# Optimization experiments

Measured on AMD Instinct MI355X. Metric: run time of the kernel, lower is better.

Reference implementation:

```python
import jax, jax.numpy as jnp
import numpy as np
import math

B, S, D = 4, 2048, 1024
N_HEADS = 16
D_FF = 4096
T_DIM = 256
KEEP_RATIO = 0.7
EPS = 1e-5


def _layernorm(x):
    mu = jnp.mean(x, axis=-1, keepdims=True)
    var = jnp.mean((x - mu) ** 2, axis=-1, keepdims=True)
    return (x - mu) * jax.lax.rsqrt(var + EPS)


def _ada_ln(x, cond, W, b):
    # cond: (B, T_DIM); W: (2D, T_DIM)
    p = jax.nn.silu(cond) @ W.T + b            # (B, 2D)
    gamma, beta = jnp.split(p, 2, axis=-1)
    return _layernorm(x) * (1.0 + gamma[:, None, :]) + beta[:, None, :]


def _mha(h, in_w, in_b, out_w, out_b):
    b, s, d = h.shape
    hd = d // N_HEADS
    qkv = h @ in_w.T + in_b                     # (b, s, 3d)
    q, k, v = jnp.split(qkv, 3, axis=-1)
    def heads(t):
        return t.reshape(b, s, N_HEADS, hd).transpose(0, 2, 1, 3)
    q, k, v = heads(q), heads(k), heads(v)
    scores = jnp.einsum('bhqd,bhkd->bhqk', q, k) / math.sqrt(hd)
    attn = jax.nn.softmax(scores, axis=-1)
    o = jnp.einsum('bhqk,bhkd->bhqd', attn, v)  # (b, h, s, hd)
    o = o.transpose(0, 2, 1, 3).reshape(b, s, d)
    return o @ out_w.T + out_b


def setup_inputs() -> dict:
    key = jax.random.key(0)
    ks = jax.random.split(key, 24)
    sc = 0.02
    return {
        'x': jax.random.normal(ks[0], (B, S, D), jnp.float32),
        't_emb': jax.random.normal(ks[1], (B, T_DIM), jnp.float32),
        'tr_w1': jax.random.normal(ks[2], (32, D), jnp.float32) * sc,
        'tr_b1': jnp.zeros((32,), jnp.float32),
        'tr_w2': jax.random.normal(ks[3], (1, 32), jnp.float32) * sc,
        'tr_b2': jnp.zeros((1,), jnp.float32),
        'ln1_w': jax.random.normal(ks[4], (2 * D, T_DIM), jnp.float32) * sc,
        'ln1_b': jnp.zeros((2 * D,), jnp.float32),
        'ln2_w': jax.random.normal(ks[5], (2 * D, T_DIM), jnp.float32) * sc,
        'ln2_b': jnp.zeros((2 * D,), jnp.float32),
        'in_proj_w': jax.random.normal(ks[6], (3 * D, D), jnp.float32) * sc,
        'in_proj_b': jnp.zeros((3 * D,), jnp.float32),
        'out_w': jax.random.normal(ks[7], (D, D), jnp.float32) * sc,
        'out_b': jnp.zeros((D,), jnp.float32),
        'ffn_w1': jax.random.normal(ks[8], (D_FF, D), jnp.float32) * sc,
        'ffn_b1': jnp.zeros((D_FF,), jnp.float32),
        'ffn_w2': jax.random.normal(ks[9], (D, D_FF), jnp.float32) * sc,
        'ffn_b2': jnp.zeros((D,), jnp.float32),
        # torch inits gates to zero; use small randn so the block is non-trivial
        'gate_attn': jax.random.normal(ks[10], (1, 1, D), jnp.float32) * sc,
        'gate_ffn': jax.random.normal(ks[11], (1, 1, D), jnp.float32) * sc,
    }


def reference(x, t_emb, tr_w1, tr_b1, tr_w2, tr_b2, ln1_w, ln1_b, ln2_w, ln2_b,
              in_proj_w, in_proj_b, out_w, out_b, ffn_w1, ffn_b1, ffn_w2, ffn_b2,
              gate_attn, gate_ffn):
    b, s, d = x.shape
    num_keep = max(int(s * KEEP_RATIO), 1)

    # token importance on detached x (stop_gradient mirrors x.detach())
    xd = jax.lax.stop_gradient(x)
    imp = jax.nn.silu(xd @ tr_w1.T + tr_b1) @ tr_w2.T + tr_b2  # (b, s, 1)
    imp = imp[..., 0]
    _, idx = jax.lax.top_k(imp, num_keep)
    idx = jnp.sort(idx, axis=-1)                               # (b, num_keep)

    x_sel = jnp.take_along_axis(x, idx[..., None], axis=1)     # (b, k, d)

    h = _ada_ln(x_sel, t_emb, ln1_w, ln1_b)
    h = _mha(h, in_proj_w, in_proj_b, out_w, out_b)
    x_sel = x_sel + gate_attn * h

    h = _ada_ln(x_sel, t_emb, ln2_w, ln2_b)
    h = jax.nn.gelu(h @ ffn_w1.T + ffn_b1, approximate=False) @ ffn_w2.T + ffn_b2
    x_sel = x_sel + gate_ffn * h

    batch_idx = jnp.arange(b)[:, None]
    return x.at[batch_idx, idx].set(x_sel)
```

## Files before the change

kernel.cpp:

```cpp
#include <hip/hip_runtime.h>
#include <hip/hip_bf16.h>
#include <cmath>
#include <cstdint>

typedef __bf16 bf16;
typedef __bf16 bf16x8 __attribute__((ext_vector_type(8)));
typedef __bf16 bf16x4 __attribute__((ext_vector_type(4)));
typedef float  f32x4  __attribute__((ext_vector_type(4)));

constexpr int B_   = 4;
constexpr int S_   = 2048;
constexpr int D_   = 1024;
constexpr int H_   = 16;
constexpr int DFF_ = 4096;
constexpr int TD_  = 256;
constexpr int KEEP = 1433;
constexpr int M_TOT = B_ * KEEP;
constexpr int MPAD  = 5888;
constexpr int QT64  = (KEEP + 63) / 64;
constexpr int NKV   = (KEEP + 63) / 64;
constexpr float EPS = 1e-5f;
constexpr float QSCALE = 0.18033688011112042f;

__device__ __forceinline__ f32x4 mfma16(bf16x8 a, bf16x8 b, f32x4 c) {
  return __builtin_amdgcn_mfma_f32_16x16x32_bf16(a, b, c, 0, 0, 0);
}

#define GLOAD_LDS(gp, lp)                                                     \
  __builtin_amdgcn_global_load_lds(                                           \
      (const __attribute__((address_space(1))) void*)(gp),                    \
      (__attribute__((address_space(3))) void*)(lp), 16, 0, 0)

#define FENCE_BARRIER()                                                       \
  do {                                                                        \
    __builtin_amdgcn_sched_barrier(0);                                        \
    __builtin_amdgcn_s_barrier();                                             \
    __builtin_amdgcn_sched_barrier(0);                                        \
  } while (0)

__global__ __launch_bounds__(256) void k_impgemv(
    const float* __restrict__ x, const float* __restrict__ w1,
    double* __restrict__ hidden)
{
  const int lane = threadIdx.x & 63, w = threadIdx.x >> 6;
  const int tok0 = blockIdx.x * 16 + w * 4;
  const int u0 = blockIdx.y * 8;
  const float* xb = x + (size_t)tok0 * D_ + lane * 4;
  const float* wb = w1 + (size_t)u0 * D_ + lane * 4;
  double acc[4][8] = {};
#pragma unroll 2
  for (int c = 0; c < D_; c += 256) {
    float4 xv[4], wv[8];
#pragma unroll
    for (int i = 0; i < 4; ++i)
      xv[i] = *(const float4*)(xb + (size_t)i * D_ + c);
#pragma unroll
    for (int u = 0; u < 8; ++u)
      wv[u] = *(const float4*)(wb + (size_t)u * D_ + c);
#pragma unroll
    for (int i = 0; i < 4; ++i)
#pragma unroll
      for (int u = 0; u < 8; ++u) {
        acc[i][u] += (double)xv[i].x * (double)wv[u].x;
        acc[i][u] += (double)xv[i].y * (double)wv[u].y;
        acc[i][u] += (double)xv[i].z * (double)wv[u].z;
        acc[i][u] += (double)xv[i].w * (double)wv[u].w;
      }
  }
#pragma unroll
  for (int i = 0; i < 4; ++i)
#pragma unroll
    for (int u = 0; u < 8; ++u) {
      double s = acc[i][u];
      for (int o = 32; o > 0; o >>= 1) s += __shfl_xor(s, o);
      acc[i][u] = s;
    }
  if (lane == 0) {
#pragma unroll
    for (int i = 0; i < 4; ++i)
#pragma unroll
      for (int u = 0; u < 8; ++u)
        hidden[(size_t)(tok0 + i) * 32 + u0 + u] = acc[i][u];
  }
}

__global__ __launch_bounds__(256) void k_imptail(
    const double* __restrict__ hidden, const float* __restrict__ b1,
    const float* __restrict__ w2, const float* __restrict__ b2,
    double* __restrict__ imp)
{
  const int tok = blockIdx.x * 256 + threadIdx.x;
  const double* hp = hidden + (size_t)tok * 32;
  double r = 0.0;
#pragma unroll
  for (int u = 0; u < 32; ++u) {
    double s = hp[u] + (double)b1[u];
    double sv = s / (1.0 + exp(-s));
    r += sv * (double)w2[u];
  }
  imp[tok] = r + (double)b2[0];
}

__global__ __launch_bounds__(256) void k_rank(const double* __restrict__ imp,
                                              int* __restrict__ rank)
{
  const int b = blockIdx.x >> 5;
  const int seg = blockIdx.x & 31;
  __shared__ double vals[S_];
  const double* ib = imp + (size_t)b * S_;
  for (int i = threadIdx.x; i < S_ / 2; i += 256)
    ((double2*)vals)[i] = ((const double2*)ib)[i];
  __syncthreads();
  const int tl = threadIdx.x >> 2;
  const int part = threadIdx.x & 3;
  const int s = seg * 64 + tl;
  const double v = vals[s];
  int cnt = 0;
  for (int j = part * 512; j < (part + 1) * 512; ++j) {
    double u = vals[j];
    cnt += (u > v) || (u == v && j < s);
  }
  cnt += __shfl_xor(cnt, 1);
  cnt += __shfl_xor(cnt, 2);
  if (part == 0) rank[b * S_ + s] = cnt;
}

__global__ __launch_bounds__(256) void k_compact(const int* __restrict__ rank,
                                                 int* __restrict__ idx)
{
  const int b = blockIdx.x;
  __shared__ int wcnt[4];
  __shared__ int base_s;
  if (threadIdx.x == 0) base_s = 0;
  __syncthreads();
  const int t = threadIdx.x, lane = t & 63, w = t >> 6;
  for (int c = 0; c < S_ / 256; ++c) {
    const int s = c * 256 + t;
    const bool kept = rank[b * S_ + s] < KEEP;
    unsigned long long m = __ballot(kept);
    int piw = __popcll(m & ((1ull << lane) - 1ull));
    if (lane == 0) wcnt[w] = __popcll(m);
    __syncthreads();
    int off = base_s;
    for (int i = 0; i < w; ++i) off += wcnt[i];
    if (kept) idx[b * KEEP + off + piw] = s;
    __syncthreads();
    if (t == 0) base_s += wcnt[0] + wcnt[1] + wcnt[2] + wcnt[3];
    __syncthreads();
  }
}

__global__ __launch_bounds__(256) void k_condproj(
    const float* __restrict__ temb, const float* __restrict__ W,
    const float* __restrict__ bias, float* __restrict__ p)
{
  const int gw = (int)((blockIdx.x * 256 + threadIdx.x) >> 6);
  const int lane = threadIdx.x & 63;
  const int b = gw >> 11;
  const int row = gw & 2047;
  const float* te = temb + (size_t)b * TD_;
  const float* wr = W + (size_t)row * TD_;
  float acc = 0.f;
  for (int i = lane; i < TD_; i += 64) {
    float c = te[i];
    acc += (c / (1.f + __expf(-c))) * wr[i];
  }
  for (int o = 32; o > 0; o >>= 1) acc += __shfl_down(acc, o);
  if (lane == 0) p[(size_t)b * 2 * D_ + row] = acc + bias[row];
}

__global__ void k_f2b(const float* __restrict__ src, bf16* __restrict__ dst, int n4)
{
  int i = blockIdx.x * 256 + threadIdx.x;
  if (i < n4) {
    float4 v = ((const float4*)src)[i];
    bf16x4 o = {(bf16)v.x, (bf16)v.y, (bf16)v.z, (bf16)v.w};
    ((bf16x4*)dst)[i] = o;
  }
}

__global__ __launch_bounds__(256) void k_adaln(
    const float* __restrict__ xsrc, const int* __restrict__ idx,
    const float* __restrict__ p, bf16* __restrict__ hout)
{
  const int r = blockIdx.x, t = threadIdx.x;
  bf16* orow = hout + (size_t)r * D_;
  if (r >= M_TOT) {
    bf16x4 z = {(bf16)0.f, (bf16)0.f, (bf16)0.f, (bf16)0.f};
    ((bf16x4*)orow)[t] = z;
    return;
  }
  const int b = r / KEEP, j = r - b * KEEP;
  const int s = idx[b * KEEP + j];
  const float* xr = xsrc + ((size_t)(b * S_ + s)) * D_;
  float4 v = ((const float4*)xr)[t];
  __shared__ float red[8];
  float sum = v.x + v.y + v.z + v.w;
  for (int o = 32; o > 0; o >>= 1) sum += __shfl_down(sum, o);
  const int lane = t & 63, w = t >> 6;
  if (lane == 0) red[w] = sum;
  __syncthreads();
  const float mu = (red[0] + red[1] + red[2] + red[3]) * (1.f / D_);
  const float dx = v.x - mu, dy = v.y - mu, dz = v.z - mu, dw = v.w - mu;
  float vs = dx * dx + dy * dy + dz * dz + dw * dw;
  for (int o = 32; o > 0; o >>= 1) vs += __shfl_down(vs, o);
  if (lane == 0) red[4 + w] = vs;
  __syncthreads();
  const float rstd = rsqrtf((red[4] + red[5] + red[6] + red[7]) * (1.f / D_) + EPS);
  const float* gp = p + (size_t)b * 2 * D_;
  float4 g  = ((const float4*)gp)[t];
  float4 be = ((const float4*)(gp + D_))[t];
  bf16x4 o;
  o[0] = (bf16)(dx * rstd * (1.f + g.x) + be.x);
  o[1] = (bf16)(dy * rstd * (1.f + g.y) + be.y);
  o[2] = (bf16)(dz * rstd * (1.f + g.z) + be.z);
  o[3] = (bf16)(dw * rstd * (1.f + g.w) + be.w);
  ((bf16x4*)orow)[t] = o;
}

template <int BN, int MODE>
__global__ __launch_bounds__(256) void k_gemm(
    const bf16* __restrict__ A, const bf16* __restrict__ W,
    const float* __restrict__ bias, bf16* __restrict__ Cbf,
    const float* __restrict__ gate, const int* __restrict__ idx,
    float* __restrict__ resid, int N, int K, int gn)
{
  constexpr int WN = BN / 2;
  constexpr int NJ = WN / 16;
  __shared__ bf16 As[2][128 * 64];
  __shared__ bf16 Ws[2][BN * 64];
  const int t = threadIdx.x, lane = t & 63;
  const int w = t >> 6, wr = w >> 1, wc = w & 1;
  const int fr = lane & 15, fq = lane >> 4;

  const int nwg = gridDim.x, orig = blockIdx.x;
  const int q8 = nwg >> 3, r8 = nwg & 7;
  const int xc = orig & 7, pos = orig >> 3;
  const int wgid = (xc < r8 ? xc * (q8 + 1) : r8 * (q8 + 1) + (xc - r8) * q8) + pos;
  const int bm = wgid / gn, bn = wgid - bm * gn;

  const bf16* Ab = A + (size_t)bm * 128 * K;
  const bf16* Wb = W + (size_t)bn * BN * K;

  auto stage = [&](int buf, int kt) {
    const int ko = kt * 64;
#pragma unroll
    for (int it = 0; it < 4; ++it) {
      const int e = it * 256 + t;
      const int row = e >> 3, pc = e & 7;
      const int lc = pc ^ (row & 7);
      GLOAD_LDS(Ab + (size_t)row * K + ko + lc * 8, &As[buf][0] + e * 8);
    }
#pragma unroll
    for (int it = 0; it < BN / 32; ++it) {
      const int e = it * 256 + t;
      const int row = e >> 3, pc = e & 7;
      const int lc = pc ^ (row & 7);
      GLOAD_LDS(Wb + (size_t)row * K + ko + lc * 8, &Ws[buf][0] + e * 8);
    }
  };

  f32x4 acc[4][NJ] = {};
  stage(0, 0);
  const int nkt = K >> 6;
  int cur = 0;
  for (int kt = 0; kt < nkt; ++kt) {
    __syncthreads();
    if (kt + 1 < nkt) stage(cur ^ 1, kt + 1);
    const char* Al = (const char*)&As[cur][0];
    const char* Wl = (const char*)&Ws[cur][0];
#pragma unroll
    for (int kk = 0; kk < 2; ++kk) {
      bf16x8 af[4], wf[NJ];
#pragma unroll
      for (int i = 0; i < 4; ++i)
        af[i] = *(const bf16x8*)(Al + (wr * 64 + i * 16 + fr) * 128 +
                                 (((kk * 4 + fq) ^ (fr & 7)) << 4));
#pragma unroll
      for (int j = 0; j < NJ; ++j)
        wf[j] = *(const bf16x8*)(Wl + (wc * WN + j * 16 + fr) * 128 +
                                 (((kk * 4 + fq) ^ (fr & 7)) << 4));
#pragma unroll
      for (int i = 0; i < 4; ++i)
#pragma unroll
        for (int j = 0; j < NJ; ++j)
          acc[i][j] = mfma16(af[i], wf[j], acc[i][j]);
    }
    cur ^= 1;
  }

#pragma unroll
  for (int i = 0; i < 4; ++i) {
#pragma unroll
    for (int j = 0; j < NJ; ++j) {
#pragma unroll
      for (int r = 0; r < 4; ++r) {
        const int m = bm * 128 + wr * 64 + i * 16 + fq * 4 + r;
        const int n = bn * BN + wc * WN + j * 16 + fr;
        float v = acc[i][j][r] + bias[n];
        if (MODE == 0) {
          if (n < D_) v *= QSCALE;
          Cbf[(size_t)m * N + n] = (bf16)v;
        } else if (MODE == 1) {
          float gl = 0.5f * v * (1.f + erff(v * 0.70710678118654752f));
          Cbf[(size_t)m * N + n] = (bf16)gl;
        } else {
          if (m < M_TOT) {
            const int b = m / KEEP, jj = m - b * KEEP;
            const int s = idx[b * KEEP + jj];
            resid[((size_t)(b * S_ + s)) * D_ + n] += gate[n] * v;
          }
        }
      }
    }
  }
}

template <int MODE>
__global__ __launch_bounds__(512) void k_gemm256(
    const bf16* __restrict__ A, const bf16* __restrict__ W,
    const float* __restrict__ bias, bf16* __restrict__ Cbf, int N, int K, int gn)
{
  __shared__ bf16 As[2][256 * 64];
  __shared__ bf16 Ws[2][256 * 64];
  const int t = threadIdx.x, lane = t & 63;
  const int wid = t >> 6, wr = wid >> 2, wc = wid & 3;
  const int fr = lane & 15, fq = lane >> 4;

  const int nwg = gridDim.x, orig = blockIdx.x;
  const int q8 = nwg >> 3, r8 = nwg & 7;
  const int xc = orig & 7, pos = orig >> 3;
  const int wgid = (xc < r8 ? xc * (q8 + 1) : r8 * (q8 + 1) + (xc - r8) * q8) + pos;
  const int bm = wgid / gn, bn = wgid - bm * gn;

  const bf16* Ab = A + (size_t)bm * 256 * K;
  const bf16* Wb = W + (size_t)bn * 256 * K;

  const bf16* pA[4];
  const bf16* pW[4];
#pragma unroll
  for (int it = 0; it < 4; ++it) {
    const int e = it * 512 + t;
    const int row = e >> 3, pc = e & 7;
    const int lc = pc ^ (row & 7);
    pA[it] = Ab + (size_t)row * K + lc * 8;
    pW[it] = Wb + (size_t)row * K + lc * 8;
  }

  auto stage = [&](int buf) {
#pragma unroll
    for (int it = 0; it < 4; ++it) {
      const int e = it * 512 + t;
      GLOAD_LDS(pA[it], &As[buf][0] + e * 8);
      pA[it] += 64;
    }
#pragma unroll
    for (int it = 0; it < 4; ++it) {
      const int e = it * 512 + t;
      GLOAD_LDS(pW[it], &Ws[buf][0] + e * 8);
      pW[it] += 64;
    }
  };

  f32x4 acc[8][4] = {};
  stage(0);
  stage(1);
  const int nkt = K >> 6;

  for (int kt = 0; kt < nkt; ++kt) {
    if (kt < nkt - 1) {
      asm volatile("s_waitcnt vmcnt(8)" ::: "memory");
    } else {
      asm volatile("s_waitcnt vmcnt(0)" ::: "memory");
    }
    FENCE_BARRIER();
    const int c = kt & 1;
    const char* Al = (const char*)&As[c][0];
    const char* Wl = (const char*)&Ws[c][0];
#pragma unroll
    for (int kk = 0; kk < 2; ++kk) {
      bf16x8 af[8], wf[4];
      const int pcsel = ((kk * 4 + fq) ^ (fr & 7)) << 4;
#pragma unroll
      for (int i = 0; i < 8; ++i)
        af[i] = *(const bf16x8*)(Al + (wr * 128 + i * 16 + fr) * 128 + pcsel);
#pragma unroll
      for (int j = 0; j < 4; ++j)
        wf[j] = *(const bf16x8*)(Wl + (wc * 64 + j * 16 + fr) * 128 + pcsel);
      __builtin_amdgcn_s_setprio(1);
#pragma unroll
      for (int i = 0; i < 8; ++i)
#pragma unroll
        for (int j = 0; j < 4; ++j)
          acc[i][j] = mfma16(af[i], wf[j], acc[i][j]);
      __builtin_amdgcn_s_setprio(0);
    }
    FENCE_BARRIER();
    if (kt + 2 < nkt) stage(c);
  }

#pragma unroll
  for (int i = 0; i < 8; ++i) {
#pragma unroll
    for (int j = 0; j < 4; ++j) {
#pragma unroll
      for (int r = 0; r < 4; ++r) {
        const int m = bm * 256 + wr * 128 + i * 16 + fq * 4 + r;
        const int n = bn * 256 + wc * 64 + j * 16 + fr;
        float v = acc[i][j][r] + bias[n];
        if (MODE == 0) {
          if (n < D_) v *= QSCALE;
          Cbf[(size_t)m * N + n] = (bf16)v;
        } else {
          float gl = 0.5f * v * (1.f + erff(v * 0.70710678118654752f));
          Cbf[(size_t)m * N + n] = (bf16)gl;
        }
      }
    }
  }
}

__global__ __launch_bounds__(256) void k_attn(const bf16* __restrict__ qkv,
                                              bf16* __restrict__ out)
{
  __shared__ bf16 Klds[2][64 * 64];
  __shared__ bf16 Vlds[2][64 * 64];

  const int t = threadIdx.x;
  const int lane = t & 63, w = t >> 6;
  const int fr = lane & 15, fq = lane >> 4;
  const int qt = blockIdx.x, h = blockIdx.y, b = blockIdx.z;
  const size_t rowbase = (size_t)b * KEEP;
  const size_t RS = 3 * D_;
  const bf16* kbase = qkv + rowbase * RS + D_ + h * 64;
  const bf16* vbase = qkv + rowbase * RS + 2 * D_ + h * 64;

  const int wq0 = qt * 64 + w * 16;
  const int qrow = min(wq0 + fr, KEEP - 1);
  const bf16* qp = qkv + (rowbase + qrow) * RS + h * 64 + fq * 8;
  const bf16x8 qf0 = *(const bf16x8*)qp;
  const bf16x8 qf1 = *(const bf16x8*)(qp + 32);

  f32x4 o[4] = {};
  float mrow = -INFINITY, lrow = 0.f;

  const int p0 = t, p1 = 256 + t;
  auto kaddr = [&](int p, int kv) {
    const int row = p >> 3, c8p = p & 7;
    const int c8 = c8p ^ ((row & 7) ^ (row >> 3));
    const int gr = min(kv + row, KEEP - 1);
    return kbase + (size_t)gr * RS + c8 * 8;
  };
  auto vaddr = [&](int p, int kv) {
    const int db = p >> 7, ksub = (p >> 3) & 15, jr = (p >> 1) & 3,
              c8lo = p & 1;
    const int vrow = ksub * 4 + jr, vc8 = db * 2 + c8lo;
    const int gr = min(kv + vrow, KEEP - 1);
    return vbase + (size_t)gr * RS + vc8 * 8;
  };
  const bf16* kp0 = kaddr(p0, 0);
  const bf16* kp1 = kaddr(p1, 0);
  const bf16* vp0 = vaddr(p0, 0);
  const bf16* vp1 = vaddr(p1, 0);

  auto stage_fast = [&](int buf) {
    GLOAD_LDS(kp0, &Klds[buf][0] + p0 * 8);
    GLOAD_LDS(kp1, &Klds[buf][0] + p1 * 8);
    GLOAD_LDS(vp0, &Vlds[buf][0] + p0 * 8);
    GLOAD_LDS(vp1, &Vlds[buf][0] + p1 * 8);
    kp0 += 64 * RS; kp1 += 64 * RS; vp0 += 64 * RS; vp1 += 64 * RS;
  };
  auto stage_last = [&](int buf, int kv) {
    GLOAD_LDS(kaddr(p0, kv), &Klds[buf][0] + p0 * 8);
    GLOAD_LDS(kaddr(p1, kv), &Klds[buf][0] + p1 * 8);
    GLOAD_LDS(vaddr(p0, kv), &Vlds[buf][0] + p0 * 8);
    GLOAD_LDS(vaddr(p1, kv), &Vlds[buf][0] + p1 * 8);
  };

  stage_fast(0);
  int cur = 0;

  const unsigned vbase_lds0 =
      (unsigned)(size_t)(__attribute__((address_space(3))) bf16*)&Vlds[0][0];
  const unsigned vbase_lds1 =
      (unsigned)(size_t)(__attribute__((address_space(3))) bf16*)&Vlds[1][0];

  for (int ti = 0; ti < NKV; ++ti) {
    const int kv = ti * 64;
    __syncthreads();
    if (ti < NKV - 2) stage_fast(cur ^ 1);
    else if (ti == NKV - 2) stage_last(cur ^ 1, kv + 64);

    const char* Kl = (const char*)&Klds[cur][0];

    f32x4 sc[4];
    __builtin_amdgcn_s_setprio(1);
#pragma unroll
    for (int f = 0; f < 4; ++f) {
      const int row = ((f >> 1) << 5) + ((fr >> 2) << 3) + ((f & 1) << 1) +
                      (fr & 1) + (((fr >> 1) & 1) << 2);
      const int swz = (row & 7) ^ (row >> 3);
      const bf16x8 kf0 = *(const bf16x8*)(Kl + row * 128 + ((fq ^ swz) << 4));
      const bf16x8 kf1 =
          *(const bf16x8*)(Kl + row * 128 + (((fq ^ 4) ^ swz) << 4));
      f32x4 s = {0.f, 0.f, 0.f, 0.f};
      s = mfma16(kf0, qf0, s);
      s = mfma16(kf1, qf1, s);
      sc[f] = s;
    }
    __builtin_amdgcn_s_setprio(0);

    if (ti == NKV - 1) {
#pragma unroll
      for (int f = 0; f < 4; ++f)
#pragma unroll
        for (int r = 0; r < 4; ++r) {
          const int kl = ((f >> 1) << 5) + (fq << 3) + ((f & 1) << 1) +
                         (r & 1) + ((r >> 1) << 2);
          if (kv + kl >= KEEP) sc[f][r] = -INFINITY;
        }
    }
    float mx = sc[0][0];
#pragma unroll
    for (int f = 0; f < 4; ++f)
#pragma unroll
      for (int r = 0; r < 4; ++r) mx = fmaxf(mx, sc[f][r]);
    mx = fmaxf(mx, __shfl_xor(mx, 16));
    mx = fmaxf(mx, __shfl_xor(mx, 32));

    const bool noresc = __all(mx <= mrow + 8.f);
    const float mnew = noresc ? mrow : fmaxf(mrow, mx);
    float ps = 0.f;
    bf16 pe[4][4];
#pragma unroll
    for (int f = 0; f < 4; ++f)
#pragma unroll
      for (int r = 0; r < 4; ++r) {
        const float pv = exp2f(sc[f][r] - mnew);
        ps += pv;
        pe[f][r] = (bf16)pv;
      }
    ps += __shfl_xor(ps, 16);
    ps += __shfl_xor(ps, 32);
    if (!noresc) {
      const float fac = exp2f(mrow - mnew);
      lrow *= fac;
#pragma unroll
      for (int db = 0; db < 4; ++db) {
        o[db][0] *= fac; o[db][1] *= fac; o[db][2] *= fac; o[db][3] *= fac;
      }
      mrow = mnew;
    }
    lrow += ps;

    const bf16x8 pb[2] = {
        {pe[0][0], pe[0][1], pe[1][0], pe[1][1],
         pe[0][2], pe[0][3], pe[1][2], pe[1][3]},
        {pe[2][0], pe[2][1], pe[3][0], pe[3][1],
         pe[2][2], pe[2][3], pe[3][2], pe[3][3]}};
    const unsigned vb =
        (cur ? vbase_lds1 : vbase_lds0) + ((unsigned)fq << 7);
#pragma unroll
    for (int c = 0; c < 2; ++c) {
      const unsigned addr = vb + c * 1024;
      bf16x4 t0, t1, t2, t3, t4, t5, t6, t7;
      asm volatile(
          "ds_read_b64_tr_b16 %0, %8 offset:0\n\t"
          "ds_read_b64_tr_b16 %1, %8 offset:128\n\t"
          "ds_read_b64_tr_b16 %2, %8 offset:2048\n\t"
          "ds_read_b64_tr_b16 %3, %8 offset:2176\n\t"
          "ds_read_b64_tr_b16 %4, %8 offset:4096\n\t"
          "ds_read_b64_tr_b16 %5, %8 offset:4224\n\t"
          "ds_read_b64_tr_b16 %6, %8 offset:6144\n\t"
          "ds_read_b64_tr_b16 %7, %8 offset:6272\n\t"
          "s_waitcnt lgkmcnt(0)"
          : "=&v"(t0), "=&v"(t1), "=&v"(t2), "=&v"(t3),
            "=&v"(t4), "=&v"(t5), "=&v"(t6), "=&v"(t7)
          : "v"(addr));
      const bf16x8 vf0 = __builtin_shufflevector(t0, t1, 0, 1, 2, 3, 4, 5, 6, 7);
      const bf16x8 vf1 = __builtin_shufflevector(t2, t3, 0, 1, 2, 3, 4, 5, 6, 7);
      const bf16x8 vf2 = __builtin_shufflevector(t4, t5, 0, 1, 2, 3, 4, 5, 6, 7);
      const bf16x8 vf3 = __builtin_shufflevector(t6, t7, 0, 1, 2, 3, 4, 5, 6, 7);
      __builtin_amdgcn_s_setprio(1);
      o[0] = mfma16(vf0, pb[c], o[0]);
      o[1] = mfma16(vf1, pb[c], o[1]);
      o[2] = mfma16(vf2, pb[c], o[2]);
      o[3] = mfma16(vf3, pb[c], o[3]);
      __builtin_amdgcn_s_setprio(0);
    }
    cur ^= 1;
  }

  const int q = wq0 + fr;
  if (q < KEEP) {
    const float inv = 1.f / lrow;
#pragma unroll
    for (int db = 0; db < 4; ++db) {
      bf16x4 wv = {(bf16)(o[db][0] * inv), (bf16)(o[db][1] * inv),
                   (bf16)(o[db][2] * inv), (bf16)(o[db][3] * inv)};
      *(bf16x4*)(out + (rowbase + q) * (size_t)D_ + h * 64 + db * 16 + fq * 4) =
          wv;
    }
  }
}

extern "C" void kernel_launch(void* const* d_in, const int* in_sizes, int n_in,
                              void* d_out, int out_size, void* d_ws, size_t ws_size,
                              hipStream_t stream)
{
  (void)in_sizes; (void)n_in; (void)out_size; (void)ws_size;
  const float* x      = (const float*)d_in[0];
  const float* t_emb  = (const float*)d_in[1];
  const float* tr_w1  = (const float*)d_in[2];
  const float* tr_b1  = (const float*)d_in[3];
  const float* tr_w2  = (const float*)d_in[4];
  const float* tr_b2  = (const float*)d_in[5];
  const float* ln1_w  = (const float*)d_in[6];
  const float* ln1_b  = (const float*)d_in[7];
  const float* ln2_w  = (const float*)d_in[8];
  const float* ln2_b  = (const float*)d_in[9];
  const float* in_w   = (const float*)d_in[10];
  const float* in_b   = (const float*)d_in[11];
  const float* out_w  = (const float*)d_in[12];
  const float* out_b  = (const float*)d_in[13];
  const float* f1_w   = (const float*)d_in[14];
  const float* f1_b   = (const float*)d_in[15];
  const float* f2_w   = (const float*)d_in[16];
  const float* f2_b   = (const float*)d_in[17];
  const float* gate_a = (const float*)d_in[18];
  const float* gate_f = (const float*)d_in[19];

  char* ws = (char*)d_ws;
  size_t off = 0;
  auto alloc = [&](size_t bytes) -> char* {
    char* p = ws + off;
    off = (off + bytes + 255) & ~(size_t)255;
    return p;
  };
  double* imp  = (double*)alloc((size_t)B_ * S_ * 8);
  double* hid  = (double*)alloc((size_t)B_ * S_ * 32 * 8);
  int* rank    = (int*)alloc((size_t)B_ * S_ * 4);
  int* idx     = (int*)alloc((size_t)B_ * KEEP * 4);
  float* p1    = (float*)alloc((size_t)B_ * 2 * D_ * 4);
  float* p2    = (float*)alloc((size_t)B_ * 2 * D_ * 4);
  bf16* w_in   = (bf16*)alloc((size_t)3 * D_ * D_ * 2);
  bf16* w_out  = (bf16*)alloc((size_t)D_ * D_ * 2);
  bf16* w_f1   = (bf16*)alloc((size_t)DFF_ * D_ * 2);
  bf16* w_f2   = (bf16*)alloc((size_t)D_ * DFF_ * 2);
  bf16* h_bf   = (bf16*)alloc((size_t)MPAD * D_ * 2);
  bf16* big    = (bf16*)alloc((size_t)MPAD * (3 * D_ + D_) * 2);
  bf16* qkv    = big;
  bf16* attn   = big + (size_t)MPAD * 3 * D_;
  bf16* ffn1   = big;

  hipMemcpyAsync(d_out, x, (size_t)B_ * S_ * D_ * 4, hipMemcpyDeviceToDevice, stream);

  k_impgemv<<<dim3(B_ * S_ / 16, 4), 256, 0, stream>>>(x, tr_w1, hid);
  k_imptail<<<B_ * S_ / 256, 256, 0, stream>>>(hid, tr_b1, tr_w2, tr_b2, imp);
  k_rank<<<B_ * 32, 256, 0, stream>>>(imp, rank);
  k_compact<<<B_, 256, 0, stream>>>(rank, idx);

  k_condproj<<<(B_ * 2 * D_) / 4, 256, 0, stream>>>(t_emb, ln1_w, ln1_b, p1);
  k_condproj<<<(B_ * 2 * D_) / 4, 256, 0, stream>>>(t_emb, ln2_w, ln2_b, p2);

  k_f2b<<<(3 * D_ * D_ / 4 + 255) / 256, 256, 0, stream>>>(in_w, w_in, 3 * D_ * D_ / 4);
  k_f2b<<<(D_ * D_ / 4 + 255) / 256, 256, 0, stream>>>(out_w, w_out, D_ * D_ / 4);
  k_f2b<<<(DFF_ * D_ / 4 + 255) / 256, 256, 0, stream>>>(f1_w, w_f1, DFF_ * D_ / 4);
  k_f2b<<<(DFF_ * D_ / 4 + 255) / 256, 256, 0, stream>>>(f2_w, w_f2, DFF_ * D_ / 4);

  k_adaln<<<MPAD, 256, 0, stream>>>(x, idx, p1, h_bf);
  k_gemm256<0><<<23 * 12, 512, 0, stream>>>(
      h_bf, w_in, in_b, qkv, 3 * D_, D_, 12);
  k_attn<<<dim3(QT64, H_, B_), 256, 0, stream>>>(qkv, attn);
  k_gemm<64, 2><<<46 * 16, 256, 0, stream>>>(
      attn, w_out, out_b, nullptr, gate_a, idx, (float*)d_out, D_, D_, 16);
  k_adaln<<<MPAD, 256, 0, stream>>>((const float*)d_out, idx, p2, h_bf);
  k_gemm256<1><<<23 * 16, 512, 0, stream>>>(
      h_bf, w_f1, f1_b, ffn1, DFF_, D_, 16);
  k_gemm<64, 2><<<46 * 16, 256, 0, stream>>>(
      ffn1, w_f2, f2_b, nullptr, gate_f, idx, (float*)d_out, D_, DFF_, 16);
}
```

Before: 487.6 us.

## Interleave GEMM tile loads with MFMA quadrants in 256x256 kernel

```diff
diff --git a/kernel.cpp b/kernel.cpp
--- a/kernel.cpp
+++ b/kernel.cpp
@@ -317,7 +317,7 @@
 }
 
 template <int MODE>
-__global__ __launch_bounds__(512) void k_gemm256(
+__global__ __launch_bounds__(512, 1) void k_gemm256(
     const bf16* __restrict__ A, const bf16* __restrict__ W,
     const float* __restrict__ bias, bf16* __restrict__ Cbf, int N, int K, int gn)
 {
@@ -337,66 +337,139 @@
   const bf16* Wb = W + (size_t)bn * 256 * K;
 
   const bf16* pA[4];
-  const bf16* pW[4];
+  int dstA[4];
 #pragma unroll
   for (int it = 0; it < 4; ++it) {
     const int e = it * 512 + t;
     const int row = e >> 3, pc = e & 7;
     const int lc = pc ^ (row & 7);
     pA[it] = Ab + (size_t)row * K + lc * 8;
-    pW[it] = Wb + (size_t)row * K + lc * 8;
-  }
-
-  auto stage = [&](int buf) {
-#pragma unroll
-    for (int it = 0; it < 4; ++it) {
-      const int e = it * 512 + t;
-      GLOAD_LDS(pA[it], &As[buf][0] + e * 8);
-      pA[it] += 64;
-    }
-#pragma unroll
-    for (int it = 0; it < 4; ++it) {
-      const int e = it * 512 + t;
-      GLOAD_LDS(pW[it], &Ws[buf][0] + e * 8);
-      pW[it] += 64;
-    }
+    dstA[it] = e * 8;
+  }
+  const bf16* pW[4];
+  int dstW[4];
+#pragma unroll
+  for (int h = 0; h < 2; ++h)
+#pragma unroll
+    for (int it2 = 0; it2 < 2; ++it2) {
+      const int e2 = it2 * 512 + t;
+      const int r3 = e2 >> 3, pc = e2 & 7;
+      const int row = (r3 >> 5) * 64 + h * 32 + (r3 & 31);
+      const int lc = pc ^ (row & 7);
+      pW[h * 2 + it2] = Wb + (size_t)row * K + lc * 8;
+      dstW[h * 2 + it2] = row * 64 + pc * 8;
+    }
+
+  auto stA = [&](bf16* base, int it) {
+    GLOAD_LDS(pA[it], base + dstA[it]);
+    pA[it] += 64;
+  };
+  auto stW = [&](bf16* base, int idx) {
+    GLOAD_LDS(pW[idx], base + dstW[idx]);
+    pW[idx] += 64;
+  };
+  auto stageAll = [&](bf16* ab, bf16* wb2) {
+    stA(ab, 0); stA(ab, 1); stA(ab, 2); stA(ab, 3);
+    stW(wb2, 0); stW(wb2, 1); stW(wb2, 2); stW(wb2, 3);
   };
 
   f32x4 acc[8][4] = {};
-  stage(0);
-  stage(1);
+  stageAll(&As[0][0], &Ws[0][0]);
+  stageAll(&As[1][0], &Ws[1][0]);
+  asm volatile("s_waitcnt vmcnt(8)" ::: "memory");
+  FENCE_BARRIER();
+
   const int nkt = K >> 6;
-
   for (int kt = 0; kt < nkt; ++kt) {
-    if (kt < nkt - 1) {
-      asm volatile("s_waitcnt vmcnt(8)" ::: "memory");
-    } else {
-      asm volatile("s_waitcnt vmcnt(0)" ::: "memory");
-    }
-    FENCE_BARRIER();
     const int c = kt & 1;
     const char* Al = (const char*)&As[c][0];
     const char* Wl = (const char*)&Ws[c][0];
+    bf16* AsN = &As[c][0];
+    bf16* WsN = &Ws[c][0];
+    const bool st = (kt + 2 < nkt);
+
+    bf16x8 a_lo[2][4], a_hi[2][4], b_lo[2][2], b_hi[2][2];
+
 #pragma unroll
     for (int kk = 0; kk < 2; ++kk) {
-      bf16x8 af[8], wf[4];
-      const int pcsel = ((kk * 4 + fq) ^ (fr & 7)) << 4;
-#pragma unroll
-      for (int i = 0; i < 8; ++i)
-        af[i] = *(const bf16x8*)(Al + (wr * 128 + i * 16 + fr) * 128 + pcsel);
-#pragma unroll
-      for (int j = 0; j < 4; ++j)
-        wf[j] = *(const bf16x8*)(Wl + (wc * 64 + j * 16 + fr) * 128 + pcsel);
-      __builtin_amdgcn_s_setprio(1);
-#pragma unroll
-      for (int i = 0; i < 8; ++i)
-#pragma unroll
-        for (int j = 0; j < 4; ++j)
-          acc[i][j] = mfma16(af[i], wf[j], acc[i][j]);
-      __builtin_amdgcn_s_setprio(0);
+      const int pcs = ((kk * 4 + fq) ^ (fr & 7)) << 4;
+#pragma unroll
+      for (int i = 0; i < 4; ++i)
+        a_lo[kk][i] = *(const bf16x8*)(Al + (wr * 128 + i * 16 + fr) * 128 + pcs);
+#pragma unroll
+      for (int j = 0; j < 2; ++j)
+        b_lo[kk][j] = *(const bf16x8*)(Wl + (wc * 64 + j * 16 + fr) * 128 + pcs);
     }
     FENCE_BARRIER();
-    if (kt + 2 < nkt) stage(c);
+    __builtin_amdgcn_s_setprio(1);
+#pragma unroll
+    for (int kk = 0; kk < 2; ++kk)
+#pragma unroll
+      for (int i = 0; i < 4; ++i)
+#pragma unroll
+        for (int j = 0; j < 2; ++j)
+          acc[i][j] = mfma16(a_lo[kk][i], b_lo[kk][j], acc[i][j]);
+    __builtin_amdgcn_s_setprio(0);
+    FENCE_BARRIER();
+
+#pragma unroll
+    for (int kk = 0; kk < 2; ++kk) {
+      const int pcs = ((kk * 4 + fq) ^ (fr & 7)) << 4;
+#pragma unroll
+      for (int j = 0; j < 2; ++j)
+        b_hi[kk][j] =
+            *(const bf16x8*)(Wl + (wc * 64 + (2 + j) * 16 + fr) * 128 + pcs);
+    }
+    if (st) { stA(AsN, 0); stA(AsN, 2); }
+    FENCE_BARRIER();
+    __builtin_amdgcn_s_setprio(1);
+#pragma unroll
+    for (int kk = 0; kk < 2; ++kk)
+#pragma unroll
+      for (int i = 0; i < 4; ++i)
+#pragma unroll
+        for (int j = 0; j < 2; ++j)
+          acc[i][2 + j] = mfma16(a_lo[kk][i], b_hi[kk][j], acc[i][2 + j]);
+    __builtin_amdgcn_s_setprio(0);
+    FENCE_BARRIER();
+
+#pragma unroll
+    for (int kk = 0; kk < 2; ++kk) {
+      const int pcs = ((kk * 4 + fq) ^ (fr & 7)) << 4;
+#pragma unroll
+      for (int i = 0; i < 4; ++i)
+        a_hi[kk][i] =
+            *(const bf16x8*)(Al + (wr * 128 + (4 + i) * 16 + fr) * 128 + pcs);
+    }
+    if (st) { stW(WsN, 0); stW(WsN, 1); }
+    FENCE_BARRIER();
+    __builtin_amdgcn_s_setprio(1);
+#pragma unroll
+    for (int kk = 0; kk < 2; ++kk)
+#pragma unroll
+      for (int i = 0; i < 4; ++i)
+#pragma unroll
+        for (int j = 0; j < 2; ++j)
+          acc[4 + i][2 + j] = mfma16(a_hi[kk][i], b_hi[kk][j], acc[4 + i][2 + j]);
+    __builtin_amdgcn_s_setprio(0);
+    FENCE_BARRIER();
+
+    if (st) { stA(AsN, 1); stA(AsN, 3); stW(WsN, 2); stW(WsN, 3); }
+    FENCE_BARRIER();
+    __builtin_amdgcn_s_setprio(1);
+#pragma unroll
+    for (int kk = 0; kk < 2; ++kk)
+#pragma unroll
+      for (int i = 0; i < 4; ++i)
+#pragma unroll
+        for (int j = 0; j < 2; ++j)
+          acc[4 + i][j] = mfma16(a_hi[kk][i], b_lo[kk][j], acc[4 + i][j]);
+    __builtin_amdgcn_s_setprio(0);
+    if (kt < nkt - 2)
+      asm volatile("s_waitcnt vmcnt(8)" ::: "memory");
+    else if (kt == nkt - 2)
+      asm volatile("s_waitcnt vmcnt(0)" ::: "memory");
+    FENCE_BARRIER();
   }
 
 #pragma unroll
```

Measured after the change: 481.4 us. No clear change (-1.3%).
